# Kernel optimization log

Hardware: AMD Instinct MI355X
Metric: run time of the kernel (lower is better)

## Reference

```python
import jax, jax.numpy as jnp
import numpy as np

ALPHA = 0.2  # LeakyReLU negative slope
EPS = 1e-16


def setup_inputs() -> dict:
    key = jax.random.key(0)
    k0, k1, k2, k3 = jax.random.split(key, 4)
    N, E, F_in, F_out, HEADS = 50000, 1600000, 256, 128, 4
    H = jax.random.normal(k0, (N, F_in), dtype=jnp.float32)
    edge_index = jax.random.randint(k1, (2, E), 0, N)  # row0=src, row1=dst
    # Xavier-ish scaled params
    W = jax.random.normal(k2, (HEADS, F_out, F_in), dtype=jnp.float32) * (1.0 / np.sqrt(F_in))
    a = jax.random.normal(k3, (HEADS, 2 * F_out), dtype=jnp.float32) * 0.1
    bias = jnp.zeros((F_out,), dtype=jnp.float32)
    return {"H": H, "edge_index": edge_index, "W": W, "a": a, "bias": bias}


def reference(H, edge_index, W, a, bias):
    """GAT layer: per-head edge attention + segment softmax over src + SpMM, mean over heads.

    H: [N, F_in]; edge_index: [2, E]; W: [heads, F_out, F_in]; a: [heads, 2*F_out]; bias: [F_out]
    Note: a(concat(h_src, h_dst)) == h_src @ a[:F_out] + h_dst @ a[F_out:], so we compute the
    two per-node scores once on nodes instead of materializing the E x 2*F_out concat.
    """
    N = H.shape[0]
    heads, F_out, _ = W.shape
    src, dst = edge_index[0], edge_index[1]
    outs = []
    for h in range(heads):
        Ht = H @ W[h].T                      # [N, F_out]
        s_src = Ht @ a[h, :F_out]            # [N]
        s_dst = Ht @ a[h, F_out:]            # [N]
        e = s_src[src] + s_dst[dst]          # [E]
        e = jnp.where(e > 0, e, ALPHA * e)   # LeakyReLU
        # segment softmax over src nodes (matches scatter amax + scatter_add)
        e_max = jax.ops.segment_max(e, src, num_segments=N)    # [N], -inf for isolated nodes
        e_exp = jnp.exp(e - e_max[src])                         # [E]
        denom = jax.ops.segment_sum(e_exp, src, num_segments=N) # [N]
        attn = e_exp / (denom[src] + EPS)                       # [E]
        # sparse.mm(attention, Ht): out[i] = sum_{(i,j) in E} attn_ij * Ht[j]
        out = jax.ops.segment_sum(attn[:, None] * Ht[dst], src, num_segments=N)  # [N, F_out]
        outs.append(out)
    final = jnp.mean(jnp.stack(outs, axis=0), axis=0) + bias
    return final
```

## Files before the change

kernel.cpp:

```cpp
#include <hip/hip_runtime.h>

#define ALPHA 0.2f
#define EPS 1e-16f

static constexpr int F_IN = 256;
static constexpr int F_OUT = 128;
static constexpr int HEADS = 4;
static constexpr int COLS = HEADS * F_OUT;

typedef __bf16 bf16x8 __attribute__((ext_vector_type(8)));
typedef float f32x4 __attribute__((ext_vector_type(4)));

static __device__ __forceinline__ unsigned short f2bf(float f) {
  unsigned int u = __float_as_uint(f);
  unsigned int r = (u + 0x7FFFu + ((u >> 16) & 1u)) >> 16;
  return (unsigned short)r;
}
static __device__ __forceinline__ float bf_lo(unsigned int u) {
  return __uint_as_float(u << 16);
}
static __device__ __forceinline__ float bf_hi(unsigned int u) {
  return __uint_as_float(u & 0xFFFF0000u);
}

__global__ __launch_bounds__(256) void k_wcast(const float* __restrict__ W,
                                               unsigned short* __restrict__ Wb) {
  const int i = blockIdx.x * 256 + threadIdx.x;
  const float4 v = ((const float4*)W)[i];
  ((ushort4*)Wb)[i] = make_ushort4(f2bf(v.x), f2bf(v.y), f2bf(v.z), f2bf(v.w));
}

__global__ void k_rank(const int* __restrict__ src, int* __restrict__ cnt,
                       unsigned short* __restrict__ rank, int E) {
  int i = blockIdx.x * blockDim.x + threadIdx.x;
  const int stride = gridDim.x * blockDim.x;
  for (; i < E; i += stride) rank[i] = (unsigned short)atomicAdd(&cnt[src[i]], 1);
}

__global__ __launch_bounds__(256) void k_gemm_q(const float* __restrict__ A,
                                                const unsigned short* __restrict__ B,
                                                unsigned char* __restrict__ Hq,
                                                unsigned char* __restrict__ rec,
                                                float* __restrict__ ssrc,
                                                const float* __restrict__ Av, int N) {
  __shared__ __bf16 As[128][40];
  __shared__ __bf16 Bs[128][40];
  __shared__ float sS[128], sD[128];
  const int T = gridDim.x;
  const int q8 = T >> 3, r8 = T & 7;
  const int xcd = blockIdx.x & 7, ii = blockIdx.x >> 3;
  const int gp = (xcd < r8) ? xcd * (q8 + 1) + ii
                            : r8 * (q8 + 1) + (xcd - r8) * q8 + ii;
  const int by = gp >> 2;
  const int bx = gp & 3;
  const int t = threadIdx.x;
  const int w = t >> 6, l = t & 63;
  const int wr = w >> 1, wc = w & 1;
  const int m0 = by << 7, n0 = bx << 7;
  const int lr = t >> 1, seg16 = (t & 1) << 4;
  f32x4 acc[4][4] = {};
  for (int k0 = 0; k0 < F_IN; k0 += 32) {
    int ar = m0 + lr; if (ar >= N) ar = N - 1;
    const float4 f0 = *(const float4*)&A[(size_t)ar * F_IN + k0 + seg16];
    const float4 f1 = *(const float4*)&A[(size_t)ar * F_IN + k0 + seg16 + 4];
    const float4 f2 = *(const float4*)&A[(size_t)ar * F_IN + k0 + seg16 + 8];
    const float4 f3 = *(const float4*)&A[(size_t)ar * F_IN + k0 + seg16 + 12];
    const uint4 b0 = *(const uint4*)&B[(size_t)(n0 + lr) * F_IN + k0 + seg16];
    const uint4 b1 = *(const uint4*)&B[(size_t)(n0 + lr) * F_IN + k0 + seg16 + 8];
    bf16x8 v0, v1;
    v0[0] = (__bf16)f0.x; v0[1] = (__bf16)f0.y; v0[2] = (__bf16)f0.z; v0[3] = (__bf16)f0.w;
    v0[4] = (__bf16)f1.x; v0[5] = (__bf16)f1.y; v0[6] = (__bf16)f1.z; v0[7] = (__bf16)f1.w;
    v1[0] = (__bf16)f2.x; v1[1] = (__bf16)f2.y; v1[2] = (__bf16)f2.z; v1[3] = (__bf16)f2.w;
    v1[4] = (__bf16)f3.x; v1[5] = (__bf16)f3.y; v1[6] = (__bf16)f3.z; v1[7] = (__bf16)f3.w;
    __syncthreads();
    *(bf16x8*)&As[lr][seg16] = v0;  *(bf16x8*)&As[lr][seg16 + 8] = v1;
    *(uint4*)&Bs[lr][seg16] = b0;   *(uint4*)&Bs[lr][seg16 + 8] = b1;
    __syncthreads();
    const int kb = (l >> 4) << 3;
    bf16x8 af[4], bf_[4];
#pragma unroll
    for (int mi = 0; mi < 4; ++mi)
      af[mi] = *(const bf16x8*)&As[(wr << 6) + (mi << 4) + (l & 15)][kb];
#pragma unroll
    for (int ni = 0; ni < 4; ++ni)
      bf_[ni] = *(const bf16x8*)&Bs[(wc << 6) + (ni << 4) + (l & 15)][kb];
#pragma unroll
    for (int mi = 0; mi < 4; ++mi)
#pragma unroll
      for (int ni = 0; ni < 4; ++ni)
        acc[mi][ni] = __builtin_amdgcn_mfma_f32_16x16x32_bf16(af[mi], bf_[ni], acc[mi][ni], 0, 0, 0);
  }
  {
    float as_[4], ad_[4];
#pragma unroll
    for (int ni = 0; ni < 4; ++ni) {
      const int f = (wc << 6) + (ni << 4) + (l & 15);
      as_[ni] = Av[bx * 256 + f];
      ad_[ni] = Av[bx * 256 + 128 + f];
    }
#pragma unroll
    for (int mi = 0; mi < 4; ++mi)
#pragma unroll
      for (int r = 0; r < 4; ++r) {
        float ds_ = 0.f, dd_ = 0.f;
#pragma unroll
        for (int ni = 0; ni < 4; ++ni) {
          ds_ = fmaf(acc[mi][ni][r], as_[ni], ds_);
          dd_ = fmaf(acc[mi][ni][r], ad_[ni], dd_);
        }
#pragma unroll
        for (int m = 1; m < 16; m <<= 1) {
          ds_ += __shfl_xor(ds_, m);
          dd_ += __shfl_xor(dd_, m);
        }
        if (wc == 0 && (l & 15) == 0) {
          const int rl = (wr << 6) + (mi << 4) + ((l >> 4) << 2) + r;
          sS[rl] = ds_; sD[rl] = dd_;
        }
      }
    __syncthreads();
    if (wc == 1) {
#pragma unroll
      for (int mi = 0; mi < 4; ++mi)
#pragma unroll
        for (int r = 0; r < 4; ++r) {
          float ds_ = 0.f, dd_ = 0.f;
#pragma unroll
          for (int ni = 0; ni < 4; ++ni) {
            ds_ = fmaf(acc[mi][ni][r], as_[ni], ds_);
            dd_ = fmaf(acc[mi][ni][r], ad_[ni], dd_);
          }
#pragma unroll
          for (int m = 1; m < 16; m <<= 1) {
            ds_ += __shfl_xor(ds_, m);
            dd_ += __shfl_xor(dd_, m);
          }
          if ((l & 15) == 0) {
            const int rl = (wr << 6) + (mi << 4) + ((l >> 4) << 2) + r;
            const int row = m0 + rl;
            if (row < N) {
              ssrc[row * 4 + bx] = sS[rl] + ds_;
              *(float*)&rec[(size_t)row * 32 + (bx << 2)] = sD[rl] + dd_;
            }
          }
        }
    }
  }
  const int bxg = (bx << 1) + wc;
#pragma unroll
  for (int mi = 0; mi < 4; ++mi)
#pragma unroll
    for (int r = 0; r < 4; ++r) {
      float mx = 0.f;
#pragma unroll
      for (int ni = 0; ni < 4; ++ni) mx = fmaxf(mx, fabsf(acc[mi][ni][r]));
#pragma unroll
      for (int m = 1; m < 16; m <<= 1) mx = fmaxf(mx, __shfl_xor(mx, m));
      const int row = m0 + (wr << 6) + (mi << 4) + ((l >> 4) << 2) + r;
      if (row < N) {
        const float inv = (mx > 0.f) ? 127.f / mx : 0.f;
        if ((l & 15) == 0)
          *(unsigned short*)&rec[(size_t)row * 32 + 16 + (bxg << 1)] = f2bf(mx * (1.f / 127.f));
        unsigned int pk = 0;
#pragma unroll
        for (int ni = 0; ni < 4; ++ni) {
          float tq = fminf(fmaxf(rintf(acc[mi][ni][r] * inv), -127.f), 127.f);
          pk |= ((unsigned int)(((int)tq + 128) & 255)) << (8 * ni);
        }
        *(unsigned int*)&Hq[(size_t)row * 512 + (bxg << 6) + ((l & 15) << 2)] = pk;
      }
    }
}

__global__ __launch_bounds__(1024) void k_scan1(int* __restrict__ cnt,
                                                int* __restrict__ bsum, int N) {
  __shared__ int ws[16];
  const int t = threadIdx.x, g = blockIdx.x * 1024 + t;
  const int lane = t & 63, w = t >> 6;
  int v = (g < N) ? cnt[g] : 0;
#pragma unroll
  for (int o = 1; o < 64; o <<= 1) {
    const int y = __shfl_up(v, o);
    if (lane >= o) v += y;
  }
  if (lane == 63) ws[w] = v;
  __syncthreads();
  if (w == 0) {
    int s = (lane < 16) ? ws[lane] : 0;
#pragma unroll
    for (int o = 1; o < 16; o <<= 1) {
      const int y = __shfl_up(s, o);
      if (lane >= o) s += y;
    }
    if (lane < 16) ws[lane] = s;
  }
  __syncthreads();
  v += (w > 0) ? ws[w - 1] : 0;
  if (g < N) cnt[g] = v;
  if (t == 1023) bsum[blockIdx.x] = v;
}

__global__ __launch_bounds__(1024) void k_scan3(const int* __restrict__ part,
                                                const int* __restrict__ bsum,
                                                int* __restrict__ off, int N, int nb) {
  __shared__ int sbuf[256];
  const int t = threadIdx.x;
  if (t < 64) {
    int carry = 0;
    for (int base = 0; base < nb; base += 64) {
      int v = (base + t < nb) ? bsum[base + t] : 0;
#pragma unroll
      for (int o = 1; o < 64; o <<= 1) {
        const int y = __shfl_up(v, o);
        if (t >= o) v += y;
      }
      v += carry;
      if (base + t < nb) sbuf[base + t] = v;
      carry = __shfl(v, 63);
    }
  }
  __syncthreads();
  const int g = blockIdx.x * 1024 + t;
  if (g == 0) off[0] = 0;
  if (g < N) off[g + 1] = part[g] + (blockIdx.x ? sbuf[blockIdx.x - 1] : 0);
}

__global__ void k_scatter(const int* __restrict__ src, const int* __restrict__ dst,
                          const int* __restrict__ off, const unsigned short* __restrict__ rank,
                          unsigned short* __restrict__ csr_dst, int E) {
  int i = blockIdx.x * blockDim.x + threadIdx.x;
  const int stride = gridDim.x * blockDim.x;
  for (; i < E; i += stride)
    csr_dst[off[src[i]] + rank[i]] = (unsigned short)dst[i];
}

__global__ __launch_bounds__(256) void k_spmm(const uint2* __restrict__ Hq2,
    const float4* __restrict__ ssrc4, const unsigned char* __restrict__ rec,
    const int* __restrict__ off, const unsigned short* __restrict__ csr_dst,
    const float* __restrict__ bias, float* __restrict__ out, int N) {
  __shared__ float wbuf[4][8][72];
  __shared__ int   ibuf[4][64];
  const int wv = threadIdx.x >> 6;
  const int lane = threadIdx.x & 63;
  const int n = (blockIdx.x << 2) + wv;
  if (n >= N) return;
  const int hg = lane >> 4;
  const int b8 = lane >> 3;
  const float4 ss4 = ssrc4[n];
  float den4[4] = {};
  float acc[8] = {};
  float sw = 0.f;
  const int beg = off[n], end = off[n + 1];
  for (int c0 = beg; c0 < end; c0 += 64) {
    const int cnt = min(64, end - c0);
    if (lane < cnt) {
      const int d = csr_dst[c0 + lane];
      ibuf[wv][lane] = d << 6;
      const float4 sd4 = *(const float4*)&rec[(size_t)d * 32];
      const uint4  sc  = *(const uint4*)&rec[(size_t)d * 32 + 16];
      float e0 = ss4.x + sd4.x; e0 = fmaxf(e0, ALPHA * e0);
      float e1 = ss4.y + sd4.y; e1 = fmaxf(e1, ALPHA * e1);
      float e2 = ss4.z + sd4.z; e2 = fmaxf(e2, ALPHA * e2);
      float e3 = ss4.w + sd4.w; e3 = fmaxf(e3, ALPHA * e3);
      const float w0 = __expf(e0), w1 = __expf(e1), w2 = __expf(e2), w3 = __expf(e3);
      den4[0] += w0; den4[1] += w1; den4[2] += w2; den4[3] += w3;
      wbuf[wv][0][lane] = w0 * bf_lo(sc.x); wbuf[wv][1][lane] = w0 * bf_hi(sc.x);
      wbuf[wv][2][lane] = w1 * bf_lo(sc.y); wbuf[wv][3][lane] = w1 * bf_hi(sc.y);
      wbuf[wv][4][lane] = w2 * bf_lo(sc.z); wbuf[wv][5][lane] = w2 * bf_hi(sc.z);
      wbuf[wv][6][lane] = w3 * bf_lo(sc.w); wbuf[wv][7][lane] = w3 * bf_hi(sc.w);
    }
#pragma unroll 8
    for (int j = 0; j < cnt; ++j) {
      const float wgt = wbuf[wv][b8][j];
      const int db = ibuf[wv][j];
      const uint2 q = Hq2[db + lane];
      sw += wgt;
      acc[0] = fmaf(wgt, (float)(q.x & 0xffu),         acc[0]);
      acc[1] = fmaf(wgt, (float)((q.x >> 8) & 0xffu),  acc[1]);
      acc[2] = fmaf(wgt, (float)((q.x >> 16) & 0xffu), acc[2]);
      acc[3] = fmaf(wgt, (float)(q.x >> 24),           acc[3]);
      acc[4] = fmaf(wgt, (float)(q.y & 0xffu),         acc[4]);
      acc[5] = fmaf(wgt, (float)((q.y >> 8) & 0xffu),  acc[5]);
      acc[6] = fmaf(wgt, (float)((q.y >> 16) & 0xffu), acc[6]);
      acc[7] = fmaf(wgt, (float)(q.y >> 24),           acc[7]);
    }
  }
#pragma unroll
  for (int k = 0; k < 4; ++k)
#pragma unroll
    for (int m = 1; m < 64; m <<= 1) den4[k] += __shfl_xor(den4[k], m);
  const float r = 1.f / (den4[hg] + EPS);
  const float corr = 128.f * sw;
#pragma unroll
  for (int i = 0; i < 8; ++i) acc[i] = (acc[i] - corr) * r;
#pragma unroll
  for (int i = 0; i < 8; ++i) {
    acc[i] += __shfl_xor(acc[i], 16);
    acc[i] += __shfl_xor(acc[i], 32);
  }
  if (lane < 16) {
    const int base = ((lane >> 3) & 1) * 64 + ((lane & 7) << 1);
#pragma unroll
    for (int k = 0; k < 4; ++k) {
      const float2 b2 = *(const float2*)&bias[base + k * 16];
      *(float2*)&out[(size_t)n * F_OUT + base + k * 16] =
          make_float2(0.25f * acc[k] + b2.x, 0.25f * acc[k + 4] + b2.y);
    }
  }
}

extern "C" void kernel_launch(void* const* d_in, const int* in_sizes, int n_in,
                              void* d_out, int out_size, void* d_ws, size_t ws_size,
                              hipStream_t stream) {
  const float* H    = (const float*)d_in[0];
  const int*   ei   = (const int*)d_in[1];
  const float* W    = (const float*)d_in[2];
  const float* a    = (const float*)d_in[3];
  const float* bias = (const float*)d_in[4];
  const int N = in_sizes[0] / F_IN;
  const int E = in_sizes[1] / 2;
  const int* src = ei;
  const int* dst = ei + E;

  char* ws = (char*)d_ws;
  size_t o = 0;
  auto alloc = [&](size_t bytes) -> void* {
    void* p = ws + o;
    o = (o + bytes + 255) & ~(size_t)255;
    return p;
  };
  unsigned short* Wb  = (unsigned short*)alloc((size_t)COLS * F_IN * 2);
  unsigned char*  Hq  = (unsigned char*)alloc((size_t)N * COLS);
  float* ssrc = (float*)alloc((size_t)N * HEADS * sizeof(float));
  unsigned char* rec = (unsigned char*)alloc((size_t)N * 32);
  int*   cnt  = (int*)alloc((size_t)N * sizeof(int));
  int*   off  = (int*)alloc(((size_t)N + 1) * sizeof(int));
  unsigned short* csr = (unsigned short*)alloc((size_t)E * sizeof(unsigned short));
  unsigned short* rank = (unsigned short*)alloc((size_t)E * sizeof(unsigned short));
  const int nb = (N + 1023) / 1024;
  int*   bsum = (int*)alloc((size_t)nb * sizeof(int));

  hipMemsetAsync(cnt, 0, (size_t)N * sizeof(int), stream);

  k_wcast<<<128, 256, 0, stream>>>(W, Wb);
  k_rank<<<1024, 256, 0, stream>>>(src, cnt, rank, E);
  const int nb128 = (N + 127) / 128;
  k_gemm_q<<<4 * nb128, 256, 0, stream>>>(H, Wb, Hq, rec, ssrc, a, N);
  k_scan1<<<nb, 1024, 0, stream>>>(cnt, bsum, N);
  k_scan3<<<nb, 1024, 0, stream>>>(cnt, bsum, off, N, nb);
  k_scatter<<<1024, 256, 0, stream>>>(src, dst, off, rank, csr, E);
  k_spmm<<<(N + 3) / 4, 256, 0, stream>>>((const uint2*)Hq, (const float4*)ssrc,
                                          rec, off, csr, bias, (float*)d_out, N);
}
```

Measured before the change: 301.3 us.

## Fuse W cast and rank counting into the GEMM kernel launch

Drops the separate W-to-bf16 cast kernel: the GEMM now loads fp32 W tiles and converts them in registers. The atomic degree/rank counting kernel is folded into the same launch as 1024 extra blocks, so it runs concurrently with the GEMM. This removes two kernel launches and the Wb round trip, and lets the atomic work overlap the matmul. In exchange the GEMM reads twice the W bytes and does extra conversions on every tile.

```diff
diff --git a/kernel.cpp b/kernel.cpp
--- a/kernel.cpp
+++ b/kernel.cpp
@@ -23,30 +23,25 @@
   return __uint_as_float(u & 0xFFFF0000u);
 }
 
-__global__ __launch_bounds__(256) void k_wcast(const float* __restrict__ W,
-                                               unsigned short* __restrict__ Wb) {
-  const int i = blockIdx.x * 256 + threadIdx.x;
-  const float4 v = ((const float4*)W)[i];
-  ((ushort4*)Wb)[i] = make_ushort4(f2bf(v.x), f2bf(v.y), f2bf(v.z), f2bf(v.w));
-}
-
-__global__ void k_rank(const int* __restrict__ src, int* __restrict__ cnt,
-                       unsigned short* __restrict__ rank, int E) {
-  int i = blockIdx.x * blockDim.x + threadIdx.x;
-  const int stride = gridDim.x * blockDim.x;
-  for (; i < E; i += stride) rank[i] = (unsigned short)atomicAdd(&cnt[src[i]], 1);
-}
-
 __global__ __launch_bounds__(256) void k_gemm_q(const float* __restrict__ A,
-                                                const unsigned short* __restrict__ B,
+                                                const float* __restrict__ Wf,
                                                 unsigned char* __restrict__ Hq,
                                                 unsigned char* __restrict__ rec,
                                                 float* __restrict__ ssrc,
-                                                const float* __restrict__ Av, int N) {
+                                                const float* __restrict__ Av, int N, int Tg,
+                                                const int* __restrict__ src,
+                                                int* __restrict__ cnt,
+                                                unsigned short* __restrict__ rank, int E) {
+  if ((int)blockIdx.x >= Tg) {
+    int i = ((int)blockIdx.x - Tg) * 256 + threadIdx.x;
+    const int stride = 1024 * 256;
+    for (; i < E; i += stride) rank[i] = (unsigned short)atomicAdd(&cnt[src[i]], 1);
+    return;
+  }
   __shared__ __bf16 As[128][40];
   __shared__ __bf16 Bs[128][40];
   __shared__ float sS[128], sD[128];
-  const int T = gridDim.x;
+  const int T = Tg;
   const int q8 = T >> 3, r8 = T & 7;
   const int xcd = blockIdx.x & 7, ii = blockIdx.x >> 3;
   const int gp = (xcd < r8) ? xcd * (q8 + 1) + ii
@@ -65,16 +60,22 @@
     const float4 f1 = *(const float4*)&A[(size_t)ar * F_IN + k0 + seg16 + 4];
     const float4 f2 = *(const float4*)&A[(size_t)ar * F_IN + k0 + seg16 + 8];
     const float4 f3 = *(const float4*)&A[(size_t)ar * F_IN + k0 + seg16 + 12];
-    const uint4 b0 = *(const uint4*)&B[(size_t)(n0 + lr) * F_IN + k0 + seg16];
-    const uint4 b1 = *(const uint4*)&B[(size_t)(n0 + lr) * F_IN + k0 + seg16 + 8];
-    bf16x8 v0, v1;
+    const float4 g0 = *(const float4*)&Wf[(size_t)(n0 + lr) * F_IN + k0 + seg16];
+    const float4 g1 = *(const float4*)&Wf[(size_t)(n0 + lr) * F_IN + k0 + seg16 + 4];
+    const float4 g2 = *(const float4*)&Wf[(size_t)(n0 + lr) * F_IN + k0 + seg16 + 8];
+    const float4 g3 = *(const float4*)&Wf[(size_t)(n0 + lr) * F_IN + k0 + seg16 + 12];
+    bf16x8 v0, v1, u0, u1;
     v0[0] = (__bf16)f0.x; v0[1] = (__bf16)f0.y; v0[2] = (__bf16)f0.z; v0[3] = (__bf16)f0.w;
     v0[4] = (__bf16)f1.x; v0[5] = (__bf16)f1.y; v0[6] = (__bf16)f1.z; v0[7] = (__bf16)f1.w;
     v1[0] = (__bf16)f2.x; v1[1] = (__bf16)f2.y; v1[2] = (__bf16)f2.z; v1[3] = (__bf16)f2.w;
     v1[4] = (__bf16)f3.x; v1[5] = (__bf16)f3.y; v1[6] = (__bf16)f3.z; v1[7] = (__bf16)f3.w;
+    u0[0] = (__bf16)g0.x; u0[1] = (__bf16)g0.y; u0[2] = (__bf16)g0.z; u0[3] = (__bf16)g0.w;
+    u0[4] = (__bf16)g1.x; u0[5] = (__bf16)g1.y; u0[6] = (__bf16)g1.z; u0[7] = (__bf16)g1.w;
+    u1[0] = (__bf16)g2.x; u1[1] = (__bf16)g2.y; u1[2] = (__bf16)g2.z; u1[3] = (__bf16)g2.w;
+    u1[4] = (__bf16)g3.x; u1[5] = (__bf16)g3.y; u1[6] = (__bf16)g3.z; u1[7] = (__bf16)g3.w;
     __syncthreads();
     *(bf16x8*)&As[lr][seg16] = v0;  *(bf16x8*)&As[lr][seg16 + 8] = v1;
-    *(uint4*)&Bs[lr][seg16] = b0;   *(uint4*)&Bs[lr][seg16 + 8] = b1;
+    *(bf16x8*)&Bs[lr][seg16] = u0;  *(bf16x8*)&Bs[lr][seg16 + 8] = u1;
     __syncthreads();
     const int kb = (l >> 4) << 3;
     bf16x8 af[4], bf_[4];
@@ -329,7 +330,6 @@
     o = (o + bytes + 255) & ~(size_t)255;
     return p;
   };
-  unsigned short* Wb  = (unsigned short*)alloc((size_t)COLS * F_IN * 2);
   unsigned char*  Hq  = (unsigned char*)alloc((size_t)N * COLS);
   float* ssrc = (float*)alloc((size_t)N * HEADS * sizeof(float));
   unsigned char* rec = (unsigned char*)alloc((size_t)N * 32);
@@ -342,10 +342,10 @@
 
   hipMemsetAsync(cnt, 0, (size_t)N * sizeof(int), stream);
 
-  k_wcast<<<128, 256, 0, stream>>>(W, Wb);
-  k_rank<<<1024, 256, 0, stream>>>(src, cnt, rank, E);
   const int nb128 = (N + 127) / 128;
-  k_gemm_q<<<4 * nb128, 256, 0, stream>>>(H, Wb, Hq, rec, ssrc, a, N);
+  const int Tg = 4 * nb128;
+  k_gemm_q<<<Tg + 1024, 256, 0, stream>>>(H, W, Hq, rec, ssrc, a, N, Tg,
+                                          src, cnt, rank, E);
   k_scan1<<<nb, 1024, 0, stream>>>(cnt, bsum, N);
   k_scan3<<<nb, 1024, 0, stream>>>(cnt, bsum, off, N, nb);
   k_scatter<<<1024, 256, 0, stream>>>(src, dst, off, rank, csr, E);
```

Result: faster. 289.6 us (-3.9%).
